# Optimization experiments

Measured on AMD Instinct MI355X. Metric: run time of the kernel, lower is better.

Reference implementation:

```python
import jax, jax.numpy as jnp
import numpy as np

BIG = jnp.float32(9e15)


def _normalize(sim, mask):
    # min/max are taken over positions where mask == 0 (faithful to the torch code)
    mn = jnp.min(jnp.where(mask == 0.0, sim, BIG), axis=-1, keepdims=True)
    mx = jnp.max(jnp.where(mask == 0.0, sim, -BIG), axis=-1, keepdims=True)
    return (sim - mn) / (mx - mn)


def setup_inputs() -> dict:
    key = jax.random.key(0)
    k1, k2 = jax.random.split(key)
    B, M = 4096, 8192
    return {
        "similarity_matrix": jax.random.normal(k1, (B, B), dtype=jnp.float32),
        "memory_bank_matrix": jax.random.normal(k2, (B, M), dtype=jnp.float32),
        "num_neighbors": 32,
        "temperature": jnp.ones((), dtype=jnp.float32),
    }


def reference(similarity_matrix, memory_bank_matrix, num_neighbors, temperature):
    sim = similarity_matrix
    B = sim.shape[0]
    eye = jnp.eye(B, dtype=sim.dtype)

    # --- neighbor masks via top-k over off-diagonal similarities ---
    sim_noself = jnp.where(eye == 0.0, sim, -BIG)
    _, topk_idx = jax.lax.top_k(sim_noself, num_neighbors)       # [B, k]
    rows = jnp.broadcast_to(jnp.arange(B)[:, None], topk_idx.shape)
    neighbor_mask = jnp.zeros((B, B), dtype=sim.dtype).at[rows, topk_idx].set(1.0)
    extended_mask = eye.at[rows, topk_idx].set(1.0)

    # --- centrality from memory bank ---
    centrality = jnp.mean(memory_bank_matrix, axis=-1)           # [B]
    cent_exp = jnp.broadcast_to(centrality[None, :], (B, B))

    norm_sim = _normalize(sim, extended_mask)
    norm_cent = _normalize(cent_exp, extended_mask)

    adjusted = jnp.where(neighbor_mask == 1.0, norm_sim - norm_cent, -BIG)

    # --- positive weights ---
    pw = jax.nn.softmax(adjusted * temperature, axis=-1)
    pw = jnp.where(neighbor_mask == 1.0, pw, 0.0)
    pw = jnp.where(eye == 1.0, 1.0, pw)  # fill_diagonal_(1.0)

    # --- masked log-softmax loss ---
    masked_sim = jnp.where(extended_mask == 1.0, sim, -BIG)
    logp = jax.nn.log_softmax(masked_sim, axis=-1) * pw
    per_row = -jnp.sum(logp, axis=-1) / jnp.sum(pw, axis=-1)
    return jnp.mean(per_row)
```

## Files before the change

### kernel.cpp

```cpp
#include <hip/hip_runtime.h>
#include <cmath>


#define CAPW 128
#define MAXIT 40

__device__ inline float wave_max_f(float x) {
#pragma unroll
    for (int off = 32; off > 0; off >>= 1) x = fmaxf(x, __shfl_xor(x, off, 64));
    return x;
}
__device__ inline float wave_min_f(float x) {
#pragma unroll
    for (int off = 32; off > 0; off >>= 1) x = fminf(x, __shfl_xor(x, off, 64));
    return x;
}
__device__ inline float wave_sum_f(float x) {
#pragma unroll
    for (int off = 32; off > 0; off >>= 1) x += __shfl_xor(x, off, 64);
    return x;
}
__device__ inline unsigned int wave_min_u32(unsigned int x) {
#pragma unroll
    for (int off = 32; off > 0; off >>= 1) {
        unsigned int o = (unsigned int)__shfl_xor((int)x, off, 64);
        x = (o < x) ? o : x;
    }
    return x;
}
__device__ inline unsigned int wave_max_u32(unsigned int x) {
#pragma unroll
    for (int off = 32; off > 0; off >>= 1) {
        unsigned int o = (unsigned int)__shfl_xor((int)x, off, 64);
        x = (o > x) ? o : x;
    }
    return x;
}

__device__ inline unsigned int f_to_key(float f) {
    unsigned int u = __float_as_uint(f);
    return u ^ ((u & 0x80000000u) ? 0xFFFFFFFFu : 0x80000000u);
}
__device__ inline float key_to_f(unsigned int key) {
    unsigned int u = key ^ ((key & 0x80000000u) ? 0x80000000u : 0xFFFFFFFFu);
    return __uint_as_float(u);
}

__device__ inline unsigned int lane_prefix(unsigned long long mask) {
    return __builtin_amdgcn_mbcnt_hi((unsigned int)(mask >> 32),
           __builtin_amdgcn_mbcnt_lo((unsigned int)mask, 0u));
}

__global__ __launch_bounds__(256)
void cent_kernel(const float* __restrict__ mem, float* __restrict__ cent, int M) {
    __shared__ float s[4];
    const int row = blockIdx.x;
    const float4* p = (const float4*)(mem + (size_t)row * M);
    const int n4 = M >> 2;
    float acc = 0.0f;
    int i = threadIdx.x;
    for (; i + 1792 < n4; i += 2048) {
        float4 q0 = p[i], q1 = p[i + 256], q2 = p[i + 512], q3 = p[i + 768];
        float4 q4 = p[i + 1024], q5 = p[i + 1280], q6 = p[i + 1536], q7 = p[i + 1792];
        acc += ((q0.x + q0.y) + (q0.z + q0.w)) + ((q1.x + q1.y) + (q1.z + q1.w))
             + ((q2.x + q2.y) + (q2.z + q2.w)) + ((q3.x + q3.y) + (q3.z + q3.w))
             + ((q4.x + q4.y) + (q4.z + q4.w)) + ((q5.x + q5.y) + (q5.z + q5.w))
             + ((q6.x + q6.y) + (q6.z + q6.w)) + ((q7.x + q7.y) + (q7.z + q7.w));
    }
    for (; i < n4; i += 256) {
        float4 q = p[i];
        acc += (q.x + q.y) + (q.z + q.w);
    }
    acc = wave_sum_f(acc);
    const int lane = threadIdx.x & 63, wid = threadIdx.x >> 6;
    if (lane == 0) s[wid] = acc;
    __syncthreads();
    if (threadIdx.x == 0) cent[row] = (s[0] + s[1] + s[2] + s[3]) / (float)M;
}

__global__ __launch_bounds__(256)
void row_loss_kernel(const float* __restrict__ sim,
                     const float* __restrict__ cent,
                     const int* __restrict__ knn,
                     const float* __restrict__ temp_p,
                     float* __restrict__ per_row, int B) {
    __shared__ __align__(16) unsigned long long cand[4][CAPW];
    __shared__ __align__(16) unsigned long long ssel[4][64];

    const int tid = threadIdx.x, lane = tid & 63, wid = tid >> 6;
    const int row = (blockIdx.x << 2) + wid;
    const int   k    = knn[0];
    const float temp = temp_p[0];
    const unsigned int uk = (unsigned int)k, need = uk + 1u;

    const float4* rp = (const float4*)(sim + (size_t)row * B);
    const float4* cp = (const float4*)cent;
    unsigned long long* mycand = cand[wid];
    unsigned long long* mysel  = ssel[wid];

    float cmin, cmax, dval;
    unsigned int kmin, wcnt;

    auto pass = [&](unsigned int kT, bool wr) {
        cmin = INFINITY; cmax = -INFINITY;
        kmin = 0xFFFFFFFFu; dval = -INFINITY; wcnt = 0u;
        for (int g = 0; g < 4; ++g) {
            float4 sv[4], cw4[4];
#pragma unroll
            for (int u = 0; u < 4; ++u) sv[u] = rp[(g * 4 + u) * 64 + lane];
#pragma unroll
            for (int u = 0; u < 4; ++u) cw4[u] = cp[(g * 4 + u) * 64 + lane];
#pragma unroll
            for (int u = 0; u < 4; ++u) {
                const int c = g * 4 + u;
                const float tv[4] = {sv[u].x, sv[u].y, sv[u].z, sv[u].w};
                const float cw[4] = {cw4[u].x, cw4[u].y, cw4[u].z, cw4[u].w};
#pragma unroll
                for (int m = 0; m < 4; ++m) {
                    const int j = c * 256 + lane * 4 + m;
                    unsigned int key = f_to_key(tv[m]);
                    const bool isd = (j == row);
                    if (isd) { dval = tv[m]; key = 0u; }
                    else if (key < kmin) kmin = key;
                    const bool p = (key > kT);
                    const unsigned long long mask = __ballot(p);
                    if (p) {
                        if (wr) {
                            const unsigned int pos = wcnt + lane_prefix(mask);
                            if (pos < CAPW)
                                mycand[pos] = ((unsigned long long)key << 32) |
                                    (unsigned long long)(0xFFFFFFFFu - (unsigned int)j);
                        }
                    } else if (!isd) {
                        cmin = fminf(cmin, cw[m]);
                        cmax = fmaxf(cmax, cw[m]);
                    }
                    wcnt += (unsigned int)__popcll(mask);
                }
            }
        }
    };

    unsigned int keyT = f_to_key(2.2f);
    pass(keyT, true);
    unsigned int n = wcnt;
    if (n < need || n > CAPW) {
        unsigned int loK = 0u, hiK = 0xFFFFFFFFu;
        for (int it = 0; it < MAXIT; ++it) {
            if (n < need) { hiK = keyT; keyT = loK + ((keyT - loK) >> 1); }
            else          { loK = keyT; keyT = keyT + ((hiK - keyT) >> 1); }
            pass(keyT, false);
            n = wcnt;
            if (n >= need && n <= CAPW) break;
        }
        pass(keyT, true);
        n = wcnt;
        if (n > CAPW) n = CAPW;
    }

    const unsigned int kminb = wave_min_u32(kmin);
    const float sdiag = wave_max_f(dval);
    const float cminP = wave_min_f(cmin);
    const float cmaxP = wave_max_f(cmax);

    __builtin_amdgcn_wave_barrier();

    unsigned long long own = mycand[lane];
    unsigned long long own2 = 0ull;
    unsigned int r = 0, r2 = 0;
    const ulonglong2* c2 = (const ulonglong2*)mycand;
    if (n <= 64u) {
#pragma unroll
        for (int o = 0; o < 32; ++o) {
            const ulonglong2 pr = c2[o];
            if ((unsigned int)(2 * o)     < n && pr.x > own) ++r;
            if ((unsigned int)(2 * o + 1) < n && pr.y > own) ++r;
        }
    } else {
        own2 = mycand[64 + lane];
#pragma unroll
        for (int o = 0; o < 64; ++o) {
            const ulonglong2 pr = c2[o];
            if ((unsigned int)(2 * o) < n) {
                if (pr.x > own)  ++r;
                if (pr.x > own2) ++r2;
            }
            if ((unsigned int)(2 * o + 1) < n) {
                if (pr.y > own)  ++r;
                if (pr.y > own2) ++r2;
            }
        }
    }

    float cmin2 = INFINITY, cmax2 = -INFINITY;
    unsigned int p33k = 0u;
    if ((unsigned int)lane < n) {
        if (r < uk) mysel[r] = own;
        else if (r == uk) p33k = (unsigned int)(own >> 32);
        if (r >= uk) {
            const int jj = (int)(0xFFFFFFFFu - (unsigned int)own);
            const float cv = cent[jj];
            cmin2 = fminf(cmin2, cv);
            cmax2 = fmaxf(cmax2, cv);
        }
    }
    if (n > 64u) {
        const unsigned int t2 = (unsigned int)lane + 64u;
        if (t2 < n) {
            if (r2 < uk) mysel[r2] = own2;
            else if (r2 == uk) p33k = (unsigned int)(own2 >> 32);
            if (r2 >= uk) {
                const int jj = (int)(0xFFFFFFFFu - (unsigned int)own2);
                const float cv = cent[jj];
                cmin2 = fminf(cmin2, cv);
                cmax2 = fmaxf(cmax2, cv);
            }
        }
    }
    p33k  = wave_max_u32(p33k);
    cmin2 = wave_min_f(cmin2);
    cmax2 = wave_max_f(cmax2);
    __builtin_amdgcn_wave_barrier();

    const float mn_c = fminf(cmin2, cminP);
    const float mx_c = fmaxf(cmax2, cmaxP);
    const float mn_s = key_to_f(kminb);
    const float mx_s = key_to_f(p33k);

    const bool act = (lane < k);
    const unsigned long long sel = act ? mysel[lane] : 0ull;
    const float sj = act ? key_to_f((unsigned int)(sel >> 32)) : -INFINITY;
    const int   j  = act ? (int)(0xFFFFFFFFu - (unsigned int)sel) : 0;
    const float cj = cent[j];

    float a = -INFINITY;
    if (act) {
        const float ns = (sj - mn_s) / (mx_s - mn_s);
        const float nc = (cj - mn_c) / (mx_c - mn_c);
        a = (ns - nc) * temp;
    }
    const float am   = wave_max_f(a);
    const float e    = act ? expf(a - am) : 0.0f;
    const float esum = wave_sum_f(e);
    const float pw   = e / esum;

    const float m2  = fmaxf(key_to_f((unsigned int)(mysel[0] >> 32)), sdiag);
    const float ex  = act ? expf(sj - m2) : 0.0f;
    const float lse = m2 + logf(wave_sum_f(ex) + expf(sdiag - m2));

    const float num = wave_sum_f(act ? pw * (sj - lse) : 0.0f) + (sdiag - lse);
    const float den = 1.0f + wave_sum_f(pw);
    if (lane == 0) per_row[row] = -num / den;
}

__global__ __launch_bounds__(256)
void reduce_kernel(const float* __restrict__ per_row, float* __restrict__ out, int B) {
    __shared__ float s[4];
    float acc = 0.0f;
    const float4* p = (const float4*)per_row;
    const int n4 = B >> 2;
    for (int i = threadIdx.x; i < n4; i += 256) {
        float4 q = p[i];
        acc += (q.x + q.y) + (q.z + q.w);
    }
    acc = wave_sum_f(acc);
    const int lane = threadIdx.x & 63, wid = threadIdx.x >> 6;
    if (lane == 0) s[wid] = acc;
    __syncthreads();
    if (threadIdx.x == 0) out[0] = (s[0] + s[1] + s[2] + s[3]) / (float)B;
}

extern "C" void kernel_launch(void* const* d_in, const int* in_sizes, int n_in,
                              void* d_out, int out_size, void* d_ws, size_t ws_size,
                              hipStream_t stream) {
    const float* sim  = (const float*)d_in[0];
    const float* mem  = (const float*)d_in[1];
    const int*   knn  = (const int*)d_in[2];
    const float* temp = (const float*)d_in[3];
    float* out     = (float*)d_out;
    float* cent    = (float*)d_ws;
    float* per_row = (float*)d_ws + 4096;

    const int B = (int)(std::sqrt((double)in_sizes[0]) + 0.5);
    const int M = in_sizes[1] / B;

    cent_kernel<<<B, 256, 0, stream>>>(mem, cent, M);
    row_loss_kernel<<<B / 4, 256, 0, stream>>>(sim, cent, knn, temp, per_row, B);
    reduce_kernel<<<1, 256, 0, stream>>>(per_row, out, B);
}
```

Measured before the change: 49.88 us.

## Precompute global centrality min/max candidate lists instead of per-row scans

Adds a single-block kernel that finds the 64 smallest and 64 largest centrality values once. Each row then takes its masked min/max from these lists, excluding its own neighbors and diagonal through a shared-memory bitmap, so the per-row pass no longer streams the whole cent vector alongside the similarity row. This removes about half the global loads in the hot pass. The cost is an extra serial kernel launch and an assumption that excluding at most k+1 entries leaves a valid value among 64; the search threshold 0.0198 is tuned to the expected centrality distribution.

```diff
diff --git a/kernel.cpp b/kernel.cpp
--- a/kernel.cpp
+++ b/kernel.cpp
@@ -4,6 +4,7 @@
 
 #define CAPW 128
 #define MAXIT 40
+#define NLIST 64
 
 __device__ inline float wave_max_f(float x) {
 #pragma unroll
@@ -79,13 +80,76 @@
 }
 
 __global__ __launch_bounds__(256)
+void centlist_kernel(const float* __restrict__ cent,
+                     unsigned long long* __restrict__ minlist,
+                     unsigned long long* __restrict__ maxlist, int B) {
+    __shared__ __align__(16) unsigned long long cand[256];
+    __shared__ unsigned int s_cnt;
+    const int tid = threadIdx.x;
+    const float4* cp = (const float4*)cent;
+    float4 v0 = cp[tid], v1 = cp[256 + tid], v2 = cp[512 + tid], v3 = cp[768 + tid];
+    float vals[16] = {v0.x, v0.y, v0.z, v0.w, v1.x, v1.y, v1.z, v1.w,
+                      v2.x, v2.y, v2.z, v2.w, v3.x, v3.y, v3.z, v3.w};
+
+    for (int side = 0; side < 2; ++side) {
+        unsigned int keys[16];
+#pragma unroll
+        for (int e = 0; e < 16; ++e) {
+            const unsigned int kk = f_to_key(vals[e]);
+            keys[e] = side ? kk : ~kk;
+        }
+        unsigned int keyT = side ? f_to_key(0.0198f) : ~f_to_key(-0.0198f);
+        unsigned int loK = 0u, hiK = 0xFFFFFFFFu, cnt = 0;
+        for (int it = 0; it < MAXIT; ++it) {
+            __syncthreads();
+            if (tid == 0) s_cnt = 0;
+            __syncthreads();
+#pragma unroll
+            for (int e = 0; e < 16; ++e) {
+                if (keys[e] > keyT) {
+                    const unsigned int pos = atomicAdd(&s_cnt, 1u);
+                    if (pos < 256u) {
+                        const unsigned int j =
+                            (unsigned int)((e >> 2) * 1024 + tid * 4 + (e & 3));
+                        cand[pos] = ((unsigned long long)keys[e] << 32) |
+                                    (unsigned long long)(0xFFFFFFFFu - j);
+                    }
+                }
+            }
+            __syncthreads();
+            cnt = s_cnt;
+            if (cnt >= (unsigned int)NLIST && cnt <= 256u) break;
+            if (cnt < (unsigned int)NLIST) { hiK = keyT; keyT = loK + ((keyT - loK) >> 1); }
+            else                           { loK = keyT; keyT = keyT + ((hiK - keyT) >> 1); }
+        }
+        const unsigned int n = min(cnt, 256u);
+        unsigned long long own = 0ull;
+        if ((unsigned int)tid < n) own = cand[tid];
+        unsigned int r = 0;
+        for (unsigned int i = 0; i < n; ++i) r += (cand[i] > own) ? 1u : 0u;
+        if ((unsigned int)tid < n && r < (unsigned int)NLIST) {
+            const unsigned int kbits = (unsigned int)(own >> 32);
+            const float val = key_to_f(side ? kbits : ~kbits);
+            const unsigned int idx = 0xFFFFFFFFu - (unsigned int)own;
+            (side ? maxlist : minlist)[r] =
+                ((unsigned long long)__float_as_uint(val) << 32) |
+                (unsigned long long)idx;
+        }
+        __syncthreads();
+    }
+}
+
+__global__ __launch_bounds__(256)
 void row_loss_kernel(const float* __restrict__ sim,
                      const float* __restrict__ cent,
+                     const unsigned long long* __restrict__ minlist,
+                     const unsigned long long* __restrict__ maxlist,
                      const int* __restrict__ knn,
                      const float* __restrict__ temp_p,
                      float* __restrict__ per_row, int B) {
     __shared__ __align__(16) unsigned long long cand[4][CAPW];
     __shared__ __align__(16) unsigned long long ssel[4][64];
+    __shared__ unsigned int bm[4][128];
 
     const int tid = threadIdx.x, lane = tid & 63, wid = tid >> 6;
     const int row = (blockIdx.x << 2) + wid;
@@ -94,46 +158,36 @@
     const unsigned int uk = (unsigned int)k, need = uk + 1u;
 
     const float4* rp = (const float4*)(sim + (size_t)row * B);
-    const float4* cp = (const float4*)cent;
     unsigned long long* mycand = cand[wid];
     unsigned long long* mysel  = ssel[wid];
-
-    float cmin, cmax, dval;
+    unsigned int*       mybm   = bm[wid];
+
+    float dval;
     unsigned int kmin, wcnt;
 
     auto pass = [&](unsigned int kT, bool wr) {
-        cmin = INFINITY; cmax = -INFINITY;
         kmin = 0xFFFFFFFFu; dval = -INFINITY; wcnt = 0u;
-        for (int g = 0; g < 4; ++g) {
-            float4 sv[4], cw4[4];
-#pragma unroll
-            for (int u = 0; u < 4; ++u) sv[u] = rp[(g * 4 + u) * 64 + lane];
-#pragma unroll
-            for (int u = 0; u < 4; ++u) cw4[u] = cp[(g * 4 + u) * 64 + lane];
-#pragma unroll
-            for (int u = 0; u < 4; ++u) {
-                const int c = g * 4 + u;
+        for (int g = 0; g < 2; ++g) {
+            float4 sv[8];
+#pragma unroll
+            for (int u = 0; u < 8; ++u) sv[u] = rp[(g * 8 + u) * 64 + lane];
+#pragma unroll
+            for (int u = 0; u < 8; ++u) {
                 const float tv[4] = {sv[u].x, sv[u].y, sv[u].z, sv[u].w};
-                const float cw[4] = {cw4[u].x, cw4[u].y, cw4[u].z, cw4[u].w};
 #pragma unroll
                 for (int m = 0; m < 4; ++m) {
-                    const int j = c * 256 + lane * 4 + m;
+                    const int j = (g * 8 + u) * 256 + lane * 4 + m;
                     unsigned int key = f_to_key(tv[m]);
                     const bool isd = (j == row);
                     if (isd) { dval = tv[m]; key = 0u; }
                     else if (key < kmin) kmin = key;
                     const bool p = (key > kT);
                     const unsigned long long mask = __ballot(p);
-                    if (p) {
-                        if (wr) {
-                            const unsigned int pos = wcnt + lane_prefix(mask);
-                            if (pos < CAPW)
-                                mycand[pos] = ((unsigned long long)key << 32) |
-                                    (unsigned long long)(0xFFFFFFFFu - (unsigned int)j);
-                        }
-                    } else if (!isd) {
-                        cmin = fminf(cmin, cw[m]);
-                        cmax = fmaxf(cmax, cw[m]);
+                    if (p && wr) {
+                        const unsigned int pos = wcnt + lane_prefix(mask);
+                        if (pos < CAPW)
+                            mycand[pos] = ((unsigned long long)key << 32) |
+                                (unsigned long long)(0xFFFFFFFFu - (unsigned int)j);
                     }
                     wcnt += (unsigned int)__popcll(mask);
                 }
@@ -160,9 +214,8 @@
 
     const unsigned int kminb = wave_min_u32(kmin);
     const float sdiag = wave_max_f(dval);
-    const float cminP = wave_min_f(cmin);
-    const float cmaxP = wave_max_f(cmax);
-
+
+    mybm[lane] = 0u; mybm[lane + 64] = 0u;
     __builtin_amdgcn_wave_barrier();
 
     unsigned long long own = mycand[lane];
@@ -192,38 +245,42 @@
         }
     }
 
-    float cmin2 = INFINITY, cmax2 = -INFINITY;
     unsigned int p33k = 0u;
     if ((unsigned int)lane < n) {
-        if (r < uk) mysel[r] = own;
-        else if (r == uk) p33k = (unsigned int)(own >> 32);
-        if (r >= uk) {
-            const int jj = (int)(0xFFFFFFFFu - (unsigned int)own);
-            const float cv = cent[jj];
-            cmin2 = fminf(cmin2, cv);
-            cmax2 = fmaxf(cmax2, cv);
-        }
+        if (r < uk) {
+            mysel[r] = own;
+            const unsigned int jj = 0xFFFFFFFFu - (unsigned int)own;
+            atomicOr(&mybm[jj >> 5], 1u << (jj & 31));
+        } else if (r == uk) p33k = (unsigned int)(own >> 32);
     }
     if (n > 64u) {
         const unsigned int t2 = (unsigned int)lane + 64u;
         if (t2 < n) {
-            if (r2 < uk) mysel[r2] = own2;
-            else if (r2 == uk) p33k = (unsigned int)(own2 >> 32);
-            if (r2 >= uk) {
-                const int jj = (int)(0xFFFFFFFFu - (unsigned int)own2);
-                const float cv = cent[jj];
-                cmin2 = fminf(cmin2, cv);
-                cmax2 = fmaxf(cmax2, cv);
-            }
-        }
-    }
-    p33k  = wave_max_u32(p33k);
-    cmin2 = wave_min_f(cmin2);
-    cmax2 = wave_max_f(cmax2);
+            if (r2 < uk) {
+                mysel[r2] = own2;
+                const unsigned int jj = 0xFFFFFFFFu - (unsigned int)own2;
+                atomicOr(&mybm[jj >> 5], 1u << (jj & 31));
+            } else if (r2 == uk) p33k = (unsigned int)(own2 >> 32);
+        }
+    }
+    if (lane == 0) atomicOr(&mybm[((unsigned int)row) >> 5], 1u << (row & 31));
+    p33k = wave_max_u32(p33k);
     __builtin_amdgcn_wave_barrier();
 
-    const float mn_c = fminf(cmin2, cminP);
-    const float mx_c = fmaxf(cmax2, cmaxP);
+    float mnv, mxv;
+    {
+        const unsigned long long eMin = minlist[lane];
+        const unsigned long long eMax = maxlist[lane];
+        const unsigned int iMin = (unsigned int)eMin, iMax = (unsigned int)eMax;
+        const float vMin = __uint_as_float((unsigned int)(eMin >> 32));
+        const float vMax = __uint_as_float((unsigned int)(eMax >> 32));
+        const bool exMin = (mybm[iMin >> 5] >> (iMin & 31)) & 1u;
+        const bool exMax = (mybm[iMax >> 5] >> (iMax & 31)) & 1u;
+        mnv = exMin ? INFINITY : vMin;
+        mxv = exMax ? -INFINITY : vMax;
+    }
+    const float mn_c = wave_min_f(mnv);
+    const float mx_c = wave_max_f(mxv);
     const float mn_s = key_to_f(kminb);
     const float mx_s = key_to_f(p33k);
 
@@ -277,14 +334,20 @@
     const float* mem  = (const float*)d_in[1];
     const int*   knn  = (const int*)d_in[2];
     const float* temp = (const float*)d_in[3];
-    float* out     = (float*)d_out;
-    float* cent    = (float*)d_ws;
-    float* per_row = (float*)d_ws + 4096;
+    float* out = (float*)d_out;
+
+    char* ws = (char*)d_ws;
+    float*              cent    = (float*)ws;
+    float*              per_row = (float*)(ws + 16384);
+    unsigned long long* minlist = (unsigned long long*)(ws + 32768);
+    unsigned long long* maxlist = (unsigned long long*)(ws + 33280);
 
     const int B = (int)(std::sqrt((double)in_sizes[0]) + 0.5);
     const int M = in_sizes[1] / B;
 
     cent_kernel<<<B, 256, 0, stream>>>(mem, cent, M);
-    row_loss_kernel<<<B / 4, 256, 0, stream>>>(sim, cent, knn, temp, per_row, B);
+    centlist_kernel<<<1, 256, 0, stream>>>(cent, minlist, maxlist, B);
+    row_loss_kernel<<<B / 4, 256, 0, stream>>>(sim, cent, minlist, maxlist,
+                                               knn, temp, per_row, B);
     reduce_kernel<<<1, 256, 0, stream>>>(per_row, out, B);
 }
```

New measurement: 60.38 us. 1.21x slower.
